# Performance work log

Measured on AMD Instinct MI355X. Metric: run time of the kernel, lower is better.

Reference implementation:

```python
import jax, jax.numpy as jnp
import numpy as np

N_ATOMS = 50000
N_MOTIFS = 50000
N_INC = 600000
N_GRAPHS = 512
H = 64            # h_dim / node_fea_dim
MOTIF_DIM = 94    # motif hyperedge feature dim
HOUT = 128        # hout_dim
Z_DIM = 2 * H + MOTIF_DIM  # concat dim inside CHGConv
BN_EPS = 1e-5


def seg_mean(x, idx, num):
    s = jax.ops.segment_sum(x, idx, num_segments=num)
    c = jax.ops.segment_sum(jnp.ones((x.shape[0], 1), x.dtype), idx, num_segments=num)
    return s / jnp.maximum(c, 1.0)


def setup_inputs() -> dict:
    key = jax.random.key(0)
    ks = jax.random.split(key, 12)
    inp = {}
    inp['atom_z'] = jax.random.randint(ks[0], (N_ATOMS,), 0, 101)
    inp['motif_attr'] = jax.random.normal(ks[1], (N_MOTIFS, MOTIF_DIM), dtype=jnp.float32)
    inp['hyperedge_index'] = jax.random.randint(ks[2], (2, N_INC), 0, N_ATOMS)
    inp['batch'] = jnp.sort(jax.random.randint(ks[3], (N_ATOMS,), 0, N_GRAPHS))
    s = 0.05
    inp['embed_table'] = jax.random.normal(ks[4], (101, H), dtype=jnp.float32) * s
    inp['w_f'] = jax.random.normal(ks[5], (Z_DIM, H), dtype=jnp.float32) * s
    inp['b_f'] = jnp.zeros((H,), jnp.float32)
    inp['w_c'] = jax.random.normal(ks[6], (Z_DIM, H), dtype=jnp.float32) * s
    inp['b_c'] = jnp.zeros((H,), jnp.float32)
    inp['bn_gamma'] = jnp.ones((H,), jnp.float32)
    inp['bn_beta'] = jnp.zeros((H,), jnp.float32)
    inp['w_l1'] = jax.random.normal(ks[7], (H, HOUT), dtype=jnp.float32) * s
    inp['b_l1'] = jnp.zeros((HOUT,), jnp.float32)
    inp['w_out'] = jax.random.normal(ks[8], (HOUT, 1), dtype=jnp.float32) * s
    inp['b_out'] = jnp.zeros((1,), jnp.float32)
    return inp


def reference(atom_z, motif_attr, hyperedge_index, batch, embed_table,
              w_f, b_f, w_c, b_c, bn_gamma, bn_beta, w_l1, b_l1, w_out, b_out):
    # atom embedding lookup
    x = embed_table[atom_z]                       # [N_ATOMS, H]
    src = hyperedge_index[0]                      # atom indices per incidence
    hid = hyperedge_index[1]                      # motif hyperedge indices per incidence

    # CHGConv: aggregate node feats to hyperedges, gated CGCNN-style message, scatter back
    hx = seg_mean(x[src], hid, N_MOTIFS)          # [N_MOTIFS, H]
    z = jnp.concatenate([x[src], hx[hid], motif_attr[hid]], axis=1)  # [N_INC, 2H+94]
    msg = jax.nn.sigmoid(z @ w_f + b_f) * jax.nn.softplus(z @ w_c + b_c)
    out = seg_mean(msg, src, N_ATOMS)             # [N_ATOMS, H]

    # batch norm (training-mode batch stats) + residual, then outer relu
    mu = out.mean(0)
    var = out.var(0)
    out = (out - mu) / jnp.sqrt(var + BN_EPS) * bn_gamma + bn_beta
    x = jax.nn.relu(out + x)

    g = seg_mean(x, batch, N_GRAPHS)              # [N_GRAPHS, H]
    h = jax.nn.softplus(g @ w_l1 + b_l1)          # [N_GRAPHS, HOUT]
    return h @ w_out + b_out                      # [N_GRAPHS, 1]
```

## Files before the change

kernel.cpp:

```cpp
#include <hip/hip_runtime.h>
#include <hip/hip_bf16.h>
#include <hip/hip_fp16.h>
#include <math.h>

#define N_ATOMS  50000
#define N_MOTIFS 50000
#define N_SEG    (N_MOTIFS + N_ATOMS)
#define N_INC    600000
#define N_GRAPHS 512
#define H        64
#define MOTIF_DIM 94
#define HOUT     128
#define BN_EPS   1e-5f
#define NZ       101
#define BCAP     64
#define NBINM    196
#define NBIN     392
#define BINCAP   4096
#define CHUNK    2048
#define NBLK_S   ((N_INC + CHUNK - 1) / CHUNK)
#define TL       32
#define NBLK_L   ((N_MOTIFS + TL - 1) / TL)
#define NBLK_P   512
#define NREP     32

__device__ __forceinline__ float softplus_fast(float x) {
    return fmaxf(x, 0.0f) + __logf(1.0f + __expf(-fabsf(x)));
}
__device__ __forceinline__ float gate_f(float f, float c) {
    float sig = __builtin_amdgcn_rcpf(1.0f + __expf(-f));
    return sig * softplus_fast(c);
}

__global__ __launch_bounds__(256) void bin_scatter(const int* __restrict__ he,
                                                   const int* __restrict__ atom_z,
                                                   unsigned* __restrict__ bin_cnt,
                                                   unsigned* __restrict__ gbin) {
    __shared__ unsigned ecnt[NBIN];
    __shared__ unsigned ebase[NBIN];
    int tid = threadIdx.x;
    int e0 = blockIdx.x * CHUNK;
    int e1 = (e0 + CHUNK < N_INC) ? e0 + CHUNK : N_INC;
    for (int i = tid; i < NBIN; i += 256) ecnt[i] = 0;
    __syncthreads();
    for (int e = e0 + tid; e < e1; e += 256) {
        int s = he[e];
        int h = he[N_INC + e];
        atomicAdd(&ecnt[h >> 8], 1u);
        atomicAdd(&ecnt[NBINM + (s >> 8)], 1u);
    }
    __syncthreads();
    for (int i = tid; i < NBIN; i += 256) {
        unsigned c = ecnt[i];
        ebase[i] = c ? atomicAdd(&bin_cnt[i], c) : 0u;
        ecnt[i] = 0u;
    }
    __syncthreads();
    for (int e = e0 + tid; e < e1; e += 256) {
        int s = he[e];
        int h = he[N_INC + e];
        int az = atom_z[s];
        int bm = h >> 8;
        unsigned sm = ebase[bm] + atomicAdd(&ecnt[bm], 1u);
        if (sm < BINCAP)
            gbin[(size_t)bm * BINCAP + sm] = ((unsigned)(h & 255) << 16) | (unsigned)az;
        int ba = NBINM + (s >> 8);
        unsigned sa = ebase[ba] + atomicAdd(&ecnt[ba], 1u);
        if (sa < BINCAP)
            gbin[(size_t)ba * BINCAP + sa] = ((unsigned)(s & 255) << 16) | (unsigned)h;
    }
}

__global__ __launch_bounds__(256) void bin_build(const unsigned* __restrict__ bin_cnt,
                                                 const unsigned* __restrict__ gbin,
                                                 unsigned* __restrict__ cnt,
                                                 unsigned char* __restrict__ csr_m,
                                                 unsigned short* __restrict__ csr_a) {
    __shared__ unsigned short bkt[256 * BCAP];
    __shared__ unsigned cnts[256];
    int b = blockIdx.x;
    int tid = threadIdx.x;
    bool isM = b < NBINM;
    int seg0 = (isM ? b : (b - NBINM)) << 8;
    int lim = 50000 - seg0; if (lim > 256) lim = 256; if (lim < 0) lim = 0;
    cnts[tid] = 0u;
    __syncthreads();
    unsigned n = bin_cnt[b];
    if (n > BINCAP) n = BINCAP;
    for (unsigned k = tid; k < n; k += 256) {
        unsigned e = gbin[(size_t)b * BINCAP + k];
        unsigned loc = e >> 16, val = e & 0xFFFFu;
        unsigned slot = atomicAdd(&cnts[loc], 1u);
        if (slot < BCAP) bkt[loc * BCAP + slot] = (unsigned short)val;
    }
    __syncthreads();
    if (tid < lim) cnt[(isM ? seg0 : N_MOTIFS + seg0) + tid] = cnts[tid];
    if (isM) {
        for (int i = tid; i < lim * 16; i += 256) {
            int loc = i >> 4, w = i & 15;
            const unsigned short* sp = &bkt[loc * BCAP + 4 * w];
            unsigned v = (sp[0] & 0xffu) | ((sp[1] & 0xffu) << 8) |
                         ((sp[2] & 0xffu) << 16) | ((sp[3] & 0xffu) << 24);
            ((unsigned*)csr_m)[(size_t)(seg0 + loc) * 16 + w] = v;
        }
    } else {
        for (int i = tid; i < lim * 32; i += 256) {
            int loc = i >> 5, w = i & 31;
            const unsigned short* sp = &bkt[loc * BCAP + 2 * w];
            unsigned v = (unsigned)sp[0] | ((unsigned)sp[1] << 16);
            ((unsigned*)csr_a)[(size_t)(seg0 + loc) * 32 + w] = v;
        }
    }
}

__global__ __launch_bounds__(256) void aux_kernel(const float* __restrict__ table,
                                                  const float* __restrict__ w_f,
                                                  const float* __restrict__ w_c,
                                                  const float* __restrict__ b_f,
                                                  const float* __restrict__ b_c,
                                                  float* __restrict__ atab_fc,
                                                  float* __restrict__ ptab_fc,
                                                  float* __restrict__ w_fc,
                                                  float* __restrict__ b_fc) {
    int t = threadIdx.x;
    int z = blockIdx.x;
    if (z >= NZ) {
        if (t < 128) {
            int sel = t & 1, col = t >> 1;
            b_fc[t] = (sel ? b_c : b_f)[col];
            const float* ws = sel ? w_c : w_f;
            for (int k = 0; k < MOTIF_DIM; k++)
                w_fc[(size_t)k * 128 + t] = ws[(size_t)(2 * H + k) * H + col];
        }
        return;
    }
    __shared__ float trow[H];
    if (t < H) trow[t] = table[(size_t)z * H + t];
    __syncthreads();
    if (t < 128) {
        int sel = (t >= 64) ? 1 : 0;
        int jj = t & 63;
        const float* ws = sel ? w_c : w_f;
        float aacc = 0.0f, pacc = 0.0f;
        for (int k = 0; k < H; k++) {
            float tv = trow[k];
            aacc += tv * ws[(size_t)k * H + jj];
            pacc += tv * ws[(size_t)(H + k) * H + jj];
        }
        atab_fc[(size_t)z * 128 + jj * 2 + sel] = aacc;
        ptab_fc[(size_t)z * 128 + jj * 2 + sel] = pacc;
    }
}

__global__ __launch_bounds__(256) void motif_gather(const unsigned* __restrict__ cnt,
                                                    const unsigned char* __restrict__ csr_m,
                                                    const float* __restrict__ ptab_fc,
                                                    const float* __restrict__ b_fc,
                                                    __half2* __restrict__ m_fc) {
    __shared__ float ptab_s[NZ * 128];
    __shared__ int   ez[TL * BCAP];
    __shared__ float invd[TL];
    __shared__ int   degs[TL];
    int tid = threadIdx.x;
    for (int k4 = tid; k4 < NZ * 32; k4 += 256)
        ((float4*)ptab_s)[k4] = ((const float4*)ptab_fc)[k4];

    int rg = tid >> 5;
    int cg = tid & 31;
    int q  = cg * 4;
    float4 bias4 = *(const float4*)(b_fc + q);

    for (int tile = blockIdx.x; tile < NBLK_L; tile += NBLK_P) {
        int m0 = tile * TL;
        __syncthreads();
        {
            const int* src = (const int*)(csr_m + (size_t)m0 * BCAP);
            for (int k = tid; k < TL * (BCAP / 4); k += 256) {
                int w = src[k];
                int b0 = k * 4;
                ez[b0]     =  w        & 0xff;
                ez[b0 + 1] = (w >> 8)  & 0xff;
                ez[b0 + 2] = (w >> 16) & 0xff;
                ez[b0 + 3] = (w >> 24) & 0xff;
            }
        }
        if (tid < TL) {
            int gm = m0 + tid;
            int d = (gm < N_MOTIFS) ? (int)cnt[gm] : 0;
            d = (d < BCAP) ? d : BCAP;
            degs[tid] = d;
            invd[tid] = 1.0f / fmaxf((float)d, 1.0f);
        }
        __syncthreads();

        float acc[4][4];
#pragma unroll
        for (int i = 0; i < 4; i++) {
            int r = rg * 4 + i;
            int lo = r * BCAP, d = degs[r];
            float g0 = 0.f, g1 = 0.f, g2 = 0.f, g3 = 0.f;
            int k = 0;
            for (; k + 8 <= d; k += 8) {
                int zz[8];
#pragma unroll
                for (int u = 0; u < 8; u++) zz[u] = ez[lo + k + u];
#pragma unroll
                for (int u = 0; u < 8; u++) {
                    float4 p = *(const float4*)(ptab_s + (zz[u] << 7) + q);
                    g0 += p.x; g1 += p.y; g2 += p.z; g3 += p.w;
                }
            }
            for (; k < d; k++) {
                float4 p = *(const float4*)(ptab_s + (ez[lo + k] << 7) + q);
                g0 += p.x; g1 += p.y; g2 += p.z; g3 += p.w;
            }
            float iv = invd[r];
            acc[i][0] = bias4.x + g0 * iv;
            acc[i][1] = bias4.y + g1 * iv;
            acc[i][2] = bias4.z + g2 * iv;
            acc[i][3] = bias4.w + g3 * iv;
        }
#pragma unroll
        for (int i = 0; i < 4; i++) {
            int gm = m0 + rg * 4 + i;
            if (gm < N_MOTIFS) {
                m_fc[(size_t)gm * 64 + cg * 2]     = __floats2half2_rn(acc[i][0], acc[i][1]);
                m_fc[(size_t)gm * 64 + cg * 2 + 1] = __floats2half2_rn(acc[i][2], acc[i][3]);
            }
        }
    }
}

__global__ __launch_bounds__(256) void motif_mm(const float* __restrict__ motif_attr,
                                                const float* __restrict__ w_fc,
                                                __half2* __restrict__ m_fc) {
    __shared__ float w_s[MOTIF_DIM * 128];
    __shared__ float z[TL][100];
    int tid = threadIdx.x;
    for (int k4 = tid; k4 < MOTIF_DIM * 32; k4 += 256)
        ((float4*)w_s)[k4] = ((const float4*)w_fc)[k4];

    int rg = tid >> 5;
    int cg = tid & 31;
    int q  = cg * 4;

    for (int tile = blockIdx.x; tile < NBLK_L; tile += NBLK_P) {
        int m0 = tile * TL;
        __syncthreads();
        for (int idx = tid; idx < TL * 47; idx += 256) {
            int m = idx / 47, k2 = idx % 47;
            int gm = m0 + m;
            float2 v = make_float2(0.f, 0.f);
            if (gm < N_MOTIFS) v = ((const float2*)motif_attr)[(size_t)gm * 47 + k2];
            *(float2*)&z[m][k2 * 2] = v;
        }
        __syncthreads();

        float2 mv0[4], mv1[4];
#pragma unroll
        for (int i = 0; i < 4; i++) {
            int gm = m0 + rg * 4 + i;
            if (gm < N_MOTIFS) {
                mv0[i] = __half22float2(m_fc[(size_t)gm * 64 + cg * 2]);
                mv1[i] = __half22float2(m_fc[(size_t)gm * 64 + cg * 2 + 1]);
            } else {
                mv0[i] = make_float2(0.f, 0.f);
                mv1[i] = make_float2(0.f, 0.f);
            }
        }

        float g[4][4];
#pragma unroll
        for (int i = 0; i < 4; i++) { g[i][0]=0.f; g[i][1]=0.f; g[i][2]=0.f; g[i][3]=0.f; }

#pragma unroll 1
        for (int k = 0; k < 92; k += 4) {
            float4 w0 = *(const float4*)(w_s + (k    ) * 128 + q);
            float4 w1 = *(const float4*)(w_s + (k + 1) * 128 + q);
            float4 w2 = *(const float4*)(w_s + (k + 2) * 128 + q);
            float4 w3 = *(const float4*)(w_s + (k + 3) * 128 + q);
#pragma unroll
            for (int i = 0; i < 4; i++) {
                float4 zv = *(const float4*)&z[rg * 4 + i][k];
                g[i][0] += zv.x * w0.x + zv.y * w1.x + zv.z * w2.x + zv.w * w3.x;
                g[i][1] += zv.x * w0.y + zv.y * w1.y + zv.z * w2.y + zv.w * w3.y;
                g[i][2] += zv.x * w0.z + zv.y * w1.z + zv.z * w2.z + zv.w * w3.z;
                g[i][3] += zv.x * w0.w + zv.y * w1.w + zv.z * w2.w + zv.w * w3.w;
            }
        }
        {
            float4 w0 = *(const float4*)(w_s + 92 * 128 + q);
            float4 w1 = *(const float4*)(w_s + 93 * 128 + q);
#pragma unroll
            for (int i = 0; i < 4; i++) {
                float2 zv = *(const float2*)&z[rg * 4 + i][92];
                g[i][0] += zv.x * w0.x + zv.y * w1.x;
                g[i][1] += zv.x * w0.y + zv.y * w1.y;
                g[i][2] += zv.x * w0.z + zv.y * w1.z;
                g[i][3] += zv.x * w0.w + zv.y * w1.w;
            }
        }
#pragma unroll
        for (int i = 0; i < 4; i++) {
            int gm = m0 + rg * 4 + i;
            if (gm < N_MOTIFS) {
                m_fc[(size_t)gm * 64 + cg * 2] =
                    __floats2half2_rn(mv0[i].x + g[i][0], mv0[i].y + g[i][1]);
                m_fc[(size_t)gm * 64 + cg * 2 + 1] =
                    __floats2half2_rn(mv1[i].x + g[i][2], mv1[i].y + g[i][3]);
            }
        }
    }
}

__global__ __launch_bounds__(256) void msg_gather(const unsigned* __restrict__ cnt,
                                                  const unsigned short* __restrict__ csr_a,
                                                  const int* __restrict__ atom_z,
                                                  const float2* __restrict__ atab_fc,
                                                  const __half2* __restrict__ m_fc,
                                                  float* __restrict__ out_mean,
                                                  float* __restrict__ bn_part) {
    int i = blockIdx.x * 4 + (threadIdx.x >> 6);
    int j = threadIdx.x & 63;
    int zi = __builtin_amdgcn_readfirstlane(atom_z[i]);
    float2 a = atab_fc[(size_t)zi * H + j];
    unsigned b = (unsigned)i * BCAP;
    int d = (int)__builtin_amdgcn_readfirstlane(cnt[N_MOTIFS + i]);
    d = (d < BCAP) ? d : BCAP;
    int dm1 = (d > 0) ? d - 1 : 0;
    float acc = 0.0f;
    for (int k = 0; k < d; k += 8) {
        int hh[8];
#pragma unroll
        for (int u = 0; u < 8; u++) {
            int o = k + u;
            hh[u] = (int)csr_a[b + (unsigned)((o < d) ? o : dm1)];
        }
        __half2 hv[8];
#pragma unroll
        for (int u = 0; u < 8; u++) hv[u] = m_fc[((unsigned)hh[u] << 6) + (unsigned)j];
#pragma unroll
        for (int u = 0; u < 8; u++)
            if (k + u < d) {
                float2 v = __half22float2(hv[u]);
                acc += gate_f(a.x + v.x, a.y + v.y);
            }
    }
    float v = acc / fmaxf((float)d, 1.0f);
    out_mean[(size_t)i * H + j] = v;
    __shared__ float ssum[256];
    __shared__ float ssq[256];
    ssum[threadIdx.x] = v; ssq[threadIdx.x] = v * v;
    __syncthreads();
    if (threadIdx.x < 64) {
        float* rep = bn_part + (size_t)(blockIdx.x & (NREP - 1)) * 128;
        atomicAdd(&rep[j],      ssum[j] + ssum[64 + j] + ssum[128 + j] + ssum[192 + j]);
        atomicAdd(&rep[64 + j], ssq[j]  + ssq[64 + j]  + ssq[128 + j]  + ssq[192 + j]);
    }
}

__global__ __launch_bounds__(256) void pool_head(const float* __restrict__ out_mean,
                                                 const float* __restrict__ bn_part,
                                                 const float* __restrict__ gamma,
                                                 const float* __restrict__ beta,
                                                 const int* __restrict__ atom_z,
                                                 const float* __restrict__ table,
                                                 const int* __restrict__ batch,
                                                 const float* __restrict__ w_l1,
                                                 const float* __restrict__ b_l1,
                                                 const float* __restrict__ w_out,
                                                 const float* __restrict__ b_out,
                                                 float* __restrict__ out) {
    int g = blockIdx.x;
    int tid = threadIdx.x;
    __shared__ int bounds[2];
    __shared__ float red[256];
    __shared__ float gv[H];
    __shared__ float red2[HOUT];
    __shared__ float bnred[128];
    if (tid < 2) {
        int target = g + tid;
        int lo = 0, hi = N_ATOMS;
        while (lo < hi) {
            int mid = (lo + hi) >> 1;
            if (batch[mid] < target) lo = mid + 1; else hi = mid;
        }
        bounds[tid] = lo;
    }
    if (tid < 128) {
        float s = 0.0f;
        for (int r = 0; r < NREP; r++) s += bn_part[(size_t)r * 128 + tid];
        bnred[tid] = s;
    }
    __syncthreads();
    int s = bounds[0], e = bounds[1];
    int j = tid & 63, w = tid >> 6;
    const float invN = 1.0f / (float)N_ATOMS;
    float mu = bnred[j] * invN;
    float var = bnred[64 + j] * invN - mu * mu;
    float rstd = 1.0f / sqrtf(var + BN_EPS);
    float gm = gamma[j], bt = beta[j];
    float acc = 0.0f;
    for (int i = s + w; i < e; i += 4) {
        float d = out_mean[(size_t)i * H + j];
        float xv = table[(size_t)atom_z[i] * H + j];
        float o = (d - mu) * rstd * gm + bt;
        acc += fmaxf(o + xv, 0.0f);
    }
    red[tid] = acc;
    __syncthreads();
    if (tid < 64)
        gv[j] = (red[j] + red[64 + j] + red[128 + j] + red[192 + j])
                / fmaxf((float)(e - s), 1.0f);
    __syncthreads();
    if (tid < HOUT) {
        float a2 = b_l1[tid];
        for (int k = 0; k < H; k++) a2 += gv[k] * w_l1[(size_t)k * HOUT + tid];
        red2[tid] = softplus_fast(a2) * w_out[tid];
    }
    __syncthreads();
    for (int st = 64; st > 0; st >>= 1) {
        if (tid < st) red2[tid] += red2[tid + st];
        __syncthreads();
    }
    if (tid == 0) out[g] = red2[0] + b_out[0];
}

extern "C" void kernel_launch(void* const* d_in, const int* in_sizes, int n_in,
                              void* d_out, int out_size, void* d_ws, size_t ws_size,
                              hipStream_t stream) {
    const int*   atom_z     = (const int*)  d_in[0];
    const float* motif_attr = (const float*)d_in[1];
    const int*   he         = (const int*)  d_in[2];
    const int*   batch      = (const int*)  d_in[3];
    const float* table      = (const float*)d_in[4];
    const float* w_f        = (const float*)d_in[5];
    const float* b_f        = (const float*)d_in[6];
    const float* w_c        = (const float*)d_in[7];
    const float* b_c        = (const float*)d_in[8];
    const float* gamma      = (const float*)d_in[9];
    const float* beta       = (const float*)d_in[10];
    const float* w_l1       = (const float*)d_in[11];
    const float* b_l1       = (const float*)d_in[12];
    const float* w_out      = (const float*)d_in[13];
    const float* b_out      = (const float*)d_in[14];
    float* out = (float*)d_out;

    float*    bn_part = (float*)d_ws;
    unsigned* bin_cnt = (unsigned*)(bn_part + NREP * 128);
    char*     zero_end = (char*)(bin_cnt + 400);
    unsigned* cnt     = (unsigned*)zero_end;
    unsigned* gbin    = cnt + N_SEG;
    unsigned char*  csr_m = (unsigned char*)(gbin + (size_t)NBIN * BINCAP);
    unsigned short* csr_a = (unsigned short*)(csr_m + (size_t)N_MOTIFS * BCAP);
    float*    atab_fc  = (float*)(csr_a + (size_t)N_ATOMS * BCAP);
    float*    ptab_fc  = atab_fc + (size_t)NZ * 128;
    float*    w_fc     = ptab_fc + (size_t)NZ * 128;
    float*    b_fc     = w_fc + (size_t)MOTIF_DIM * 128;
    __half2*  m_fc     = (__half2*)(b_fc + 128);
    float*    out_mean = (float*)(m_fc + (size_t)N_MOTIFS * 64);

    size_t zero_bytes = (size_t)(zero_end - (char*)d_ws);
    hipMemsetAsync(d_ws, 0, zero_bytes, stream);

    aux_kernel<<<NZ + 1, 256, 0, stream>>>(table, w_f, w_c, b_f, b_c,
                                           atab_fc, ptab_fc, w_fc, b_fc);
    bin_scatter<<<NBLK_S, 256, 0, stream>>>(he, atom_z, bin_cnt, gbin);
    bin_build<<<NBIN, 256, 0, stream>>>(bin_cnt, gbin, cnt, csr_m, csr_a);
    motif_gather<<<NBLK_P, 256, 0, stream>>>(cnt, csr_m, ptab_fc, b_fc, m_fc);
    motif_mm<<<NBLK_P, 256, 0, stream>>>(motif_attr, w_fc, m_fc);
    msg_gather<<<N_ATOMS / 4, 256, 0, stream>>>(cnt, csr_a, atom_z,
                                                (const float2*)atab_fc,
                                                m_fc, out_mean, bn_part);
    pool_head<<<N_GRAPHS, 256, 0, stream>>>(out_mean, bn_part, gamma, beta,
                                            atom_z, table, batch,
                                            w_l1, b_l1, w_out, b_out, out);
}
```

Measured before the change: 248.1 us.

## Use atomic tile scheduling in motif kernels and prefetch msg_gather neighbor rows

The persistent motif_gather and motif_mm kernels now pull tiles through a global atomic counter instead of a fixed grid stride, which balances load across blocks. In msg_gather each wave loads its atom's adjacency list once into registers. Indices are then broadcast with shuffles, and the next group of 8 m_fc rows is loaded before the current group is processed. This hides gather latency and removes repeated index loads. The cost is extra atomics, extra barriers per tile, and more registers held by the double-buffered rows.

```diff
diff --git a/kernel.cpp b/kernel.cpp
--- a/kernel.cpp
+++ b/kernel.cpp
@@ -156,11 +156,13 @@
                                                     const unsigned char* __restrict__ csr_m,
                                                     const float* __restrict__ ptab_fc,
                                                     const float* __restrict__ b_fc,
-                                                    __half2* __restrict__ m_fc) {
+                                                    __half2* __restrict__ m_fc,
+                                                    unsigned* __restrict__ tctr) {
     __shared__ float ptab_s[NZ * 128];
     __shared__ int   ez[TL * BCAP];
     __shared__ float invd[TL];
     __shared__ int   degs[TL];
+    __shared__ int   s_tile;
     int tid = threadIdx.x;
     for (int k4 = tid; k4 < NZ * 32; k4 += 256)
         ((float4*)ptab_s)[k4] = ((const float4*)ptab_fc)[k4];
@@ -170,9 +172,13 @@
     int q  = cg * 4;
     float4 bias4 = *(const float4*)(b_fc + q);
 
-    for (int tile = blockIdx.x; tile < NBLK_L; tile += NBLK_P) {
+    for (;;) {
+        __syncthreads();
+        if (tid == 0) s_tile = (int)atomicAdd(tctr, 1u);
+        __syncthreads();
+        int tile = s_tile;
+        if (tile >= NBLK_L) break;
         int m0 = tile * TL;
-        __syncthreads();
         {
             const int* src = (const int*)(csr_m + (size_t)m0 * BCAP);
             for (int k = tid; k < TL * (BCAP / 4); k += 256) {
@@ -233,9 +239,11 @@
 
 __global__ __launch_bounds__(256) void motif_mm(const float* __restrict__ motif_attr,
                                                 const float* __restrict__ w_fc,
-                                                __half2* __restrict__ m_fc) {
+                                                __half2* __restrict__ m_fc,
+                                                unsigned* __restrict__ tctr) {
     __shared__ float w_s[MOTIF_DIM * 128];
     __shared__ float z[TL][100];
+    __shared__ int   s_tile;
     int tid = threadIdx.x;
     for (int k4 = tid; k4 < MOTIF_DIM * 32; k4 += 256)
         ((float4*)w_s)[k4] = ((const float4*)w_fc)[k4];
@@ -244,9 +252,13 @@
     int cg = tid & 31;
     int q  = cg * 4;
 
-    for (int tile = blockIdx.x; tile < NBLK_L; tile += NBLK_P) {
+    for (;;) {
+        __syncthreads();
+        if (tid == 0) s_tile = (int)atomicAdd(tctr, 1u);
+        __syncthreads();
+        int tile = s_tile;
+        if (tile >= NBLK_L) break;
         int m0 = tile * TL;
-        __syncthreads();
         for (int idx = tid; idx < TL * 47; idx += 256) {
             int m = idx / 47, k2 = idx % 47;
             int gm = m0 + m;
@@ -328,24 +340,35 @@
     int d = (int)__builtin_amdgcn_readfirstlane(cnt[N_MOTIFS + i]);
     d = (d < BCAP) ? d : BCAP;
     int dm1 = (d > 0) ? d - 1 : 0;
+    int allidx = (int)csr_a[b + (unsigned)((j < d) ? j : dm1)];
+
+#define LOADB(kk, dst)                                                        \
+    {                                                                         \
+        _Pragma("unroll")                                                     \
+        for (int u = 0; u < 8; u++) {                                         \
+            int o = (kk) + u;                                                 \
+            o = (o < d) ? o : dm1;                                            \
+            int hsc = __builtin_amdgcn_readfirstlane(__shfl(allidx, o));      \
+            dst[u] = m_fc[(((size_t)hsc) << 6) + (unsigned)j];                \
+        }                                                                     \
+    }
+
     float acc = 0.0f;
+    __half2 cur[8];
+    if (d > 0) LOADB(0, cur);
     for (int k = 0; k < d; k += 8) {
-        int hh[8];
-#pragma unroll
-        for (int u = 0; u < 8; u++) {
-            int o = k + u;
-            hh[u] = (int)csr_a[b + (unsigned)((o < d) ? o : dm1)];
-        }
-        __half2 hv[8];
-#pragma unroll
-        for (int u = 0; u < 8; u++) hv[u] = m_fc[((unsigned)hh[u] << 6) + (unsigned)j];
+        __half2 nxt[8];
+        LOADB(k + 8, nxt);
 #pragma unroll
         for (int u = 0; u < 8; u++)
             if (k + u < d) {
-                float2 v = __half22float2(hv[u]);
+                float2 v = __half22float2(cur[u]);
                 acc += gate_f(a.x + v.x, a.y + v.y);
             }
-    }
+#pragma unroll
+        for (int u = 0; u < 8; u++) cur[u] = nxt[u];
+    }
+#undef LOADB
     float v = acc / fmaxf((float)d, 1.0f);
     out_mean[(size_t)i * H + j] = v;
     __shared__ float ssum[256];
@@ -448,7 +471,8 @@
 
     float*    bn_part = (float*)d_ws;
     unsigned* bin_cnt = (unsigned*)(bn_part + NREP * 128);
-    char*     zero_end = (char*)(bin_cnt + 400);
+    unsigned* tctr    = bin_cnt + 400;
+    char*     zero_end = (char*)(tctr + 8);
     unsigned* cnt     = (unsigned*)zero_end;
     unsigned* gbin    = cnt + N_SEG;
     unsigned char*  csr_m = (unsigned char*)(gbin + (size_t)NBIN * BINCAP);
@@ -467,8 +491,8 @@
                                            atab_fc, ptab_fc, w_fc, b_fc);
     bin_scatter<<<NBLK_S, 256, 0, stream>>>(he, atom_z, bin_cnt, gbin);
     bin_build<<<NBIN, 256, 0, stream>>>(bin_cnt, gbin, cnt, csr_m, csr_a);
-    motif_gather<<<NBLK_P, 256, 0, stream>>>(cnt, csr_m, ptab_fc, b_fc, m_fc);
-    motif_mm<<<NBLK_P, 256, 0, stream>>>(motif_attr, w_fc, m_fc);
+    motif_gather<<<NBLK_P, 256, 0, stream>>>(cnt, csr_m, ptab_fc, b_fc, m_fc, tctr);
+    motif_mm<<<NBLK_P, 256, 0, stream>>>(motif_attr, w_fc, m_fc, tctr + 1);
     msg_gather<<<N_ATOMS / 4, 256, 0, stream>>>(cnt, csr_a, atom_z,
                                                 (const float2*)atab_fc,
                                                 m_fc, out_mean, bn_part);
```

Result: slower. 261.8 us (+5.5%).

## Fuse motif gather and motif matmul into one fp16 dot2 kernel

Applied to the files above, without the earlier changes.

Merges the motif mean-gather kernel and the motif_attr projection kernel into a single kernel, so the intermediate m_fc no longer makes a global round trip and one launch is dropped. The lookup table and projection weights are stored as fp16 to halve their LDS footprint, and the 94-wide matmul uses packed fp16 dot2 instructions with fp32 accumulation. The tile shrinks from 32 to 16 motifs and the bounds checks are removed, which relies on N_MOTIFS being divisible by 16. Converting motif_attr and the weights to fp16 lowers precision.

```diff
diff --git a/kernel.cpp b/kernel.cpp
--- a/kernel.cpp
+++ b/kernel.cpp
@@ -10,6 +10,7 @@
 #define N_GRAPHS 512
 #define H        64
 #define MOTIF_DIM 94
+#define KP       47
 #define HOUT     128
 #define BN_EPS   1e-5f
 #define NZ       101
@@ -19,10 +20,15 @@
 #define BINCAP   4096
 #define CHUNK    2048
 #define NBLK_S   ((N_INC + CHUNK - 1) / CHUNK)
-#define TL       32
-#define NBLK_L   ((N_MOTIFS + TL - 1) / TL)
+#define TL       16
+#define NBLK_T   (N_MOTIFS / TL)
 #define NBLK_P   512
 #define NREP     32
+
+typedef _Float16 h2_t __attribute__((ext_vector_type(2)));
+__device__ __forceinline__ float fdot2(__half2 a, __half2 b, float c) {
+    return __builtin_amdgcn_fdot2(*(h2_t*)&a, *(h2_t*)&b, c, false);
+}
 
 __device__ __forceinline__ float softplus_fast(float x) {
     return fmaxf(x, 0.0f) + __logf(1.0f + __expf(-fabsf(x)));
@@ -119,8 +125,8 @@
                                                   const float* __restrict__ b_f,
                                                   const float* __restrict__ b_c,
                                                   float* __restrict__ atab_fc,
-                                                  float* __restrict__ ptab_fc,
-                                                  float* __restrict__ w_fc,
+                                                  __half* __restrict__ ptab_h,
+                                                  __half2* __restrict__ w2_fc,
                                                   float* __restrict__ b_fc) {
     int t = threadIdx.x;
     int z = blockIdx.x;
@@ -129,8 +135,10 @@
             int sel = t & 1, col = t >> 1;
             b_fc[t] = (sel ? b_c : b_f)[col];
             const float* ws = sel ? w_c : w_f;
-            for (int k = 0; k < MOTIF_DIM; k++)
-                w_fc[(size_t)k * 128 + t] = ws[(size_t)(2 * H + k) * H + col];
+            for (int kp = 0; kp < KP; kp++)
+                w2_fc[(size_t)kp * 128 + t] = __floats2half2_rn(
+                    ws[(size_t)(2 * H + 2 * kp) * H + col],
+                    ws[(size_t)(2 * H + 2 * kp + 1) * H + col]);
         }
         return;
     }
@@ -148,55 +156,63 @@
             pacc += tv * ws[(size_t)(H + k) * H + jj];
         }
         atab_fc[(size_t)z * 128 + jj * 2 + sel] = aacc;
-        ptab_fc[(size_t)z * 128 + jj * 2 + sel] = pacc;
-    }
-}
-
-__global__ __launch_bounds__(256) void motif_gather(const unsigned* __restrict__ cnt,
-                                                    const unsigned char* __restrict__ csr_m,
-                                                    const float* __restrict__ ptab_fc,
-                                                    const float* __restrict__ b_fc,
-                                                    __half2* __restrict__ m_fc) {
-    __shared__ float ptab_s[NZ * 128];
-    __shared__ int   ez[TL * BCAP];
-    __shared__ float invd[TL];
-    __shared__ int   degs[TL];
+        ptab_h[(size_t)z * 128 + jj * 2 + sel] = __float2half_rn(pacc);
+    }
+}
+
+__global__ __launch_bounds__(256) void motif_fused(const unsigned* __restrict__ cnt,
+                                                   const unsigned char* __restrict__ csr_m,
+                                                   const __half2* __restrict__ ptab_h,
+                                                   const float* __restrict__ motif_attr,
+                                                   const __half2* __restrict__ w2_fc,
+                                                   const float* __restrict__ b_fc,
+                                                   __half2* __restrict__ m_fc) {
+    __shared__ __half2 ptab_s[NZ * 64];
+    __shared__ __half2 w_s[KP * 128];
+    __shared__ __half2 z2[TL][KP];
+    __shared__ int     ez[TL * BCAP];
+    __shared__ float   invd[TL];
+    __shared__ int     degs[TL];
     int tid = threadIdx.x;
-    for (int k4 = tid; k4 < NZ * 32; k4 += 256)
-        ((float4*)ptab_s)[k4] = ((const float4*)ptab_fc)[k4];
+    for (int k4 = tid; k4 < NZ * 16; k4 += 256)
+        ((uint4*)ptab_s)[k4] = ((const uint4*)ptab_h)[k4];
+    for (int k4 = tid; k4 < KP * 32; k4 += 256)
+        ((uint4*)w_s)[k4] = ((const uint4*)w2_fc)[k4];
 
     int rg = tid >> 5;
     int cg = tid & 31;
     int q  = cg * 4;
     float4 bias4 = *(const float4*)(b_fc + q);
 
-    for (int tile = blockIdx.x; tile < NBLK_L; tile += NBLK_P) {
+    for (int tile = blockIdx.x; tile < NBLK_T; tile += NBLK_P) {
         int m0 = tile * TL;
         __syncthreads();
         {
             const int* src = (const int*)(csr_m + (size_t)m0 * BCAP);
-            for (int k = tid; k < TL * (BCAP / 4); k += 256) {
-                int w = src[k];
-                int b0 = k * 4;
-                ez[b0]     =  w        & 0xff;
-                ez[b0 + 1] = (w >> 8)  & 0xff;
-                ez[b0 + 2] = (w >> 16) & 0xff;
-                ez[b0 + 3] = (w >> 24) & 0xff;
-            }
+            int w = src[tid];
+            int b0 = tid * 4;
+            ez[b0]     =  w        & 0xff;
+            ez[b0 + 1] = (w >> 8)  & 0xff;
+            ez[b0 + 2] = (w >> 16) & 0xff;
+            ez[b0 + 3] = (w >> 24) & 0xff;
         }
         if (tid < TL) {
-            int gm = m0 + tid;
-            int d = (gm < N_MOTIFS) ? (int)cnt[gm] : 0;
+            int d = (int)cnt[m0 + tid];
             d = (d < BCAP) ? d : BCAP;
             degs[tid] = d;
             invd[tid] = 1.0f / fmaxf((float)d, 1.0f);
         }
+        for (int idx = tid; idx < TL * KP; idx += 256) {
+            int m = idx / KP, kp = idx % KP;
+            float2 v = ((const float2*)motif_attr)[(size_t)(m0 + m) * KP + kp];
+            z2[m][kp] = __float22half2_rn(v);
+        }
         __syncthreads();
 
-        float acc[4][4];
-#pragma unroll
-        for (int i = 0; i < 4; i++) {
-            int r = rg * 4 + i;
+        float acc[2][4];
+#pragma unroll
+        for (int i = 0; i < 2; i++) {
+            int r = rg * 2 + i;
             int lo = r * BCAP, d = degs[r];
             float g0 = 0.f, g1 = 0.f, g2 = 0.f, g3 = 0.f;
             int k = 0;
@@ -206,13 +222,17 @@
                 for (int u = 0; u < 8; u++) zz[u] = ez[lo + k + u];
 #pragma unroll
                 for (int u = 0; u < 8; u++) {
-                    float4 p = *(const float4*)(ptab_s + (zz[u] << 7) + q);
-                    g0 += p.x; g1 += p.y; g2 += p.z; g3 += p.w;
+                    uint2 pr = *(const uint2*)(ptab_s + zz[u] * 64 + cg * 2);
+                    float2 fa = __half22float2(*(__half2*)&pr.x);
+                    float2 fb = __half22float2(*(__half2*)&pr.y);
+                    g0 += fa.x; g1 += fa.y; g2 += fb.x; g3 += fb.y;
                 }
             }
             for (; k < d; k++) {
-                float4 p = *(const float4*)(ptab_s + (ez[lo + k] << 7) + q);
-                g0 += p.x; g1 += p.y; g2 += p.z; g3 += p.w;
+                uint2 pr = *(const uint2*)(ptab_s + ez[lo + k] * 64 + cg * 2);
+                float2 fa = __half22float2(*(__half2*)&pr.x);
+                float2 fb = __half22float2(*(__half2*)&pr.y);
+                g0 += fa.x; g1 += fa.y; g2 += fb.x; g3 += fb.y;
             }
             float iv = invd[r];
             acc[i][0] = bias4.x + g0 * iv;
@@ -220,95 +240,30 @@
             acc[i][2] = bias4.z + g2 * iv;
             acc[i][3] = bias4.w + g3 * iv;
         }
-#pragma unroll
-        for (int i = 0; i < 4; i++) {
-            int gm = m0 + rg * 4 + i;
-            if (gm < N_MOTIFS) {
-                m_fc[(size_t)gm * 64 + cg * 2]     = __floats2half2_rn(acc[i][0], acc[i][1]);
-                m_fc[(size_t)gm * 64 + cg * 2 + 1] = __floats2half2_rn(acc[i][2], acc[i][3]);
+
+        {
+            int r0 = rg * 2, r1 = r0 + 1;
+#pragma unroll 4
+            for (int kp = 0; kp < KP; kp++) {
+                uint4 wr = *(const uint4*)(w_s + (size_t)kp * 128 + q);
+                __half2 w0 = *(__half2*)&wr.x, w1 = *(__half2*)&wr.y;
+                __half2 w2h = *(__half2*)&wr.z, w3 = *(__half2*)&wr.w;
+                __half2 za = z2[r0][kp], zb = z2[r1][kp];
+                acc[0][0] = fdot2(za, w0,  acc[0][0]);
+                acc[0][1] = fdot2(za, w1,  acc[0][1]);
+                acc[0][2] = fdot2(za, w2h, acc[0][2]);
+                acc[0][3] = fdot2(za, w3,  acc[0][3]);
+                acc[1][0] = fdot2(zb, w0,  acc[1][0]);
+                acc[1][1] = fdot2(zb, w1,  acc[1][1]);
+                acc[1][2] = fdot2(zb, w2h, acc[1][2]);
+                acc[1][3] = fdot2(zb, w3,  acc[1][3]);
             }
         }
-    }
-}
-
-__global__ __launch_bounds__(256) void motif_mm(const float* __restrict__ motif_attr,
-                                                const float* __restrict__ w_fc,
-                                                __half2* __restrict__ m_fc) {
-    __shared__ float w_s[MOTIF_DIM * 128];
-    __shared__ float z[TL][100];
-    int tid = threadIdx.x;
-    for (int k4 = tid; k4 < MOTIF_DIM * 32; k4 += 256)
-        ((float4*)w_s)[k4] = ((const float4*)w_fc)[k4];
-
-    int rg = tid >> 5;
-    int cg = tid & 31;
-    int q  = cg * 4;
-
-    for (int tile = blockIdx.x; tile < NBLK_L; tile += NBLK_P) {
-        int m0 = tile * TL;
-        __syncthreads();
-        for (int idx = tid; idx < TL * 47; idx += 256) {
-            int m = idx / 47, k2 = idx % 47;
-            int gm = m0 + m;
-            float2 v = make_float2(0.f, 0.f);
-            if (gm < N_MOTIFS) v = ((const float2*)motif_attr)[(size_t)gm * 47 + k2];
-            *(float2*)&z[m][k2 * 2] = v;
-        }
-        __syncthreads();
-
-        float2 mv0[4], mv1[4];
-#pragma unroll
-        for (int i = 0; i < 4; i++) {
-            int gm = m0 + rg * 4 + i;
-            if (gm < N_MOTIFS) {
-                mv0[i] = __half22float2(m_fc[(size_t)gm * 64 + cg * 2]);
-                mv1[i] = __half22float2(m_fc[(size_t)gm * 64 + cg * 2 + 1]);
-            } else {
-                mv0[i] = make_float2(0.f, 0.f);
-                mv1[i] = make_float2(0.f, 0.f);
-            }
-        }
-
-        float g[4][4];
-#pragma unroll
-        for (int i = 0; i < 4; i++) { g[i][0]=0.f; g[i][1]=0.f; g[i][2]=0.f; g[i][3]=0.f; }
-
-#pragma unroll 1
-        for (int k = 0; k < 92; k += 4) {
-            float4 w0 = *(const float4*)(w_s + (k    ) * 128 + q);
-            float4 w1 = *(const float4*)(w_s + (k + 1) * 128 + q);
-            float4 w2 = *(const float4*)(w_s + (k + 2) * 128 + q);
-            float4 w3 = *(const float4*)(w_s + (k + 3) * 128 + q);
-#pragma unroll
-            for (int i = 0; i < 4; i++) {
-                float4 zv = *(const float4*)&z[rg * 4 + i][k];
-                g[i][0] += zv.x * w0.x + zv.y * w1.x + zv.z * w2.x + zv.w * w3.x;
-                g[i][1] += zv.x * w0.y + zv.y * w1.y + zv.z * w2.y + zv.w * w3.y;
-                g[i][2] += zv.x * w0.z + zv.y * w1.z + zv.z * w2.z + zv.w * w3.z;
-                g[i][3] += zv.x * w0.w + zv.y * w1.w + zv.z * w2.w + zv.w * w3.w;
-            }
-        }
-        {
-            float4 w0 = *(const float4*)(w_s + 92 * 128 + q);
-            float4 w1 = *(const float4*)(w_s + 93 * 128 + q);
-#pragma unroll
-            for (int i = 0; i < 4; i++) {
-                float2 zv = *(const float2*)&z[rg * 4 + i][92];
-                g[i][0] += zv.x * w0.x + zv.y * w1.x;
-                g[i][1] += zv.x * w0.y + zv.y * w1.y;
-                g[i][2] += zv.x * w0.z + zv.y * w1.z;
-                g[i][3] += zv.x * w0.w + zv.y * w1.w;
-            }
-        }
-#pragma unroll
-        for (int i = 0; i < 4; i++) {
-            int gm = m0 + rg * 4 + i;
-            if (gm < N_MOTIFS) {
-                m_fc[(size_t)gm * 64 + cg * 2] =
-                    __floats2half2_rn(mv0[i].x + g[i][0], mv0[i].y + g[i][1]);
-                m_fc[(size_t)gm * 64 + cg * 2 + 1] =
-                    __floats2half2_rn(mv1[i].x + g[i][2], mv1[i].y + g[i][3]);
-            }
+#pragma unroll
+        for (int i = 0; i < 2; i++) {
+            int gm = m0 + rg * 2 + i;
+            m_fc[(size_t)gm * 64 + cg * 2]     = __floats2half2_rn(acc[i][0], acc[i][1]);
+            m_fc[(size_t)gm * 64 + cg * 2 + 1] = __floats2half2_rn(acc[i][2], acc[i][3]);
         }
     }
 }
@@ -454,9 +409,9 @@
     unsigned char*  csr_m = (unsigned char*)(gbin + (size_t)NBIN * BINCAP);
     unsigned short* csr_a = (unsigned short*)(csr_m + (size_t)N_MOTIFS * BCAP);
     float*    atab_fc  = (float*)(csr_a + (size_t)N_ATOMS * BCAP);
-    float*    ptab_fc  = atab_fc + (size_t)NZ * 128;
-    float*    w_fc     = ptab_fc + (size_t)NZ * 128;
-    float*    b_fc     = w_fc + (size_t)MOTIF_DIM * 128;
+    __half*   ptab_h   = (__half*)(atab_fc + (size_t)NZ * 128);
+    __half2*  w2_fc    = (__half2*)(ptab_h + (size_t)NZ * 128);
+    float*    b_fc     = (float*)(w2_fc + (size_t)KP * 128);
     __half2*  m_fc     = (__half2*)(b_fc + 128);
     float*    out_mean = (float*)(m_fc + (size_t)N_MOTIFS * 64);
 
@@ -464,11 +419,11 @@
     hipMemsetAsync(d_ws, 0, zero_bytes, stream);
 
     aux_kernel<<<NZ + 1, 256, 0, stream>>>(table, w_f, w_c, b_f, b_c,
-                                           atab_fc, ptab_fc, w_fc, b_fc);
+                                           atab_fc, ptab_h, w2_fc, b_fc);
     bin_scatter<<<NBLK_S, 256, 0, stream>>>(he, atom_z, bin_cnt, gbin);
     bin_build<<<NBIN, 256, 0, stream>>>(bin_cnt, gbin, cnt, csr_m, csr_a);
-    motif_gather<<<NBLK_P, 256, 0, stream>>>(cnt, csr_m, ptab_fc, b_fc, m_fc);
-    motif_mm<<<NBLK_P, 256, 0, stream>>>(motif_attr, w_fc, m_fc);
+    motif_fused<<<NBLK_P, 256, 0, stream>>>(cnt, csr_m, (const __half2*)ptab_h,
+                                            motif_attr, w2_fc, b_fc, m_fc);
     msg_gather<<<N_ATOMS / 4, 256, 0, stream>>>(cnt, csr_a, atom_z,
                                                 (const float2*)atab_fc,
                                                 m_fc, out_mean, bn_part);
```

Result: faster. 229.6 us (-7.5%).
